# Optimization experiments

Measured on AMD Instinct MI355X. Metric: run time of the kernel, lower is better.

The kernel has to match this reference:

```python
import jax, jax.numpy as jnp
import numpy as np
import math

E = 1024      # embed_dim
H = 16        # n_heads
D = E // H    # head_dim
C = 64        # chunk_size
B = 4
N = 4096
EPS = 1e-5


def _ln(x, g, b):
    m = jnp.mean(x, axis=-1, keepdims=True)
    v = jnp.mean(jnp.square(x - m), axis=-1, keepdims=True)
    return (x - m) * jax.lax.rsqrt(v + EPS) * g + b


def _chunked_attention(q, k, v):
    # q, k, v: [B, H, N, D] -> sliding-window causal attention, window = 2*C
    b, h, n, d = q.shape
    pad = (-n) % C
    if pad:
        q = jnp.pad(q, ((0, 0), (0, 0), (0, pad), (0, 0)))
        k = jnp.pad(k, ((0, 0), (0, 0), (0, pad), (0, 0)))
        v = jnp.pad(v, ((0, 0), (0, 0), (0, pad), (0, 0)))
    np_ = n + pad
    nc = np_ // C
    qc = q.reshape(b, h, nc, C, d)
    kc = k.reshape(b, h, nc, C, d)
    vc = v.reshape(b, h, nc, C, d)
    # prepend a zero chunk, window = [prev_chunk ; current_chunk] -> [b,h,nc,2C,d]
    kp = jnp.pad(kc, ((0, 0), (0, 0), (1, 0), (0, 0), (0, 0)))
    vp = jnp.pad(vc, ((0, 0), (0, 0), (1, 0), (0, 0), (0, 0)))
    kw = jnp.concatenate([kp[:, :, :-1], kp[:, :, 1:]], axis=3)
    vw = jnp.concatenate([vp[:, :, :-1], vp[:, :, 1:]], axis=3)
    scale = 1.0 / math.sqrt(d)
    scores = jnp.einsum('bhncd,bhnwd->bhncw', qc, kw) * scale  # [b,h,nc,C,2C]
    # causal: position i in chunk may attend window slots j <= C + i
    i = jnp.arange(C)[:, None]
    j = jnp.arange(2 * C)[None, :]
    mask = j <= (C + i)
    scores = jnp.where(mask, scores, -jnp.inf)
    attn = jax.nn.softmax(scores, axis=-1)
    out = jnp.einsum('bhncw,bhnwd->bhncd', attn, vw)
    out = out.reshape(b, h, np_, d)
    return out[:, :, :n]


def setup_inputs() -> dict:
    key = jax.random.key(0)
    ks = jax.random.split(key, 20)
    s = 0.02
    inp = {
        'x': jax.random.normal(ks[0], (B, N, E), jnp.float32),
        'p_i_plus_1': jax.random.normal(ks[1], (B, N, E), jnp.float32),
        'wq': jax.random.normal(ks[2], (E, E), jnp.float32) * s,
        'bq': jnp.zeros((E,), jnp.float32),
        'wk': jax.random.normal(ks[3], (E, E), jnp.float32) * s,
        'bk': jnp.zeros((E,), jnp.float32),
        'wv': jax.random.normal(ks[4], (E, E), jnp.float32) * s,
        'bv': jnp.zeros((E,), jnp.float32),
        'wo': jax.random.normal(ks[5], (E, E), jnp.float32) * s,
        'bo': jnp.zeros((E,), jnp.float32),
        'w1': jax.random.normal(ks[6], (E, 4 * E), jnp.float32) * s,
        'b1': jnp.zeros((4 * E,), jnp.float32),
        'w2': jax.random.normal(ks[7], (4 * E, E), jnp.float32) * s,
        'b2': jnp.zeros((E,), jnp.float32),
        'g1': jnp.ones((E,), jnp.float32),
        'beta1': jnp.zeros((E,), jnp.float32),
        'g2': jnp.ones((E,), jnp.float32),
        'beta2': jnp.zeros((E,), jnp.float32),
    }
    return inp


def reference(x, p_i_plus_1, wq, bq, wk, bk, wv, bv, wo, bo,
              w1, b1, w2, b2, g1, beta1, g2, beta2):
    b, n, e = x.shape
    resid = x
    xn = _ln(x, g1, beta1)
    q = (xn @ wq + bq).reshape(b, n, H, D).transpose(0, 2, 1, 3)
    k = (xn @ wk + bk).reshape(b, n, H, D).transpose(0, 2, 1, 3)
    v = (xn @ wv + bv).reshape(b, n, H, D).transpose(0, 2, 1, 3)
    ao = _chunked_attention(q, k, v)               # [b,H,n,D]
    ao = ao.transpose(0, 2, 1, 3).reshape(b, n, e)
    x1 = resid + (ao @ wo + bo)
    h = _ln(x1, g2, beta2)
    ff = jax.nn.gelu(h @ w1 + b1, approximate=False) @ w2 + b2
    x2 = x1 + ff
    pc_loss = jnp.mean(jnp.square(x2 - p_i_plus_1))
    return (x2, x2, pc_loss)
```

## Files before the change

kernel.cpp:

```cpp
#include <hip/hip_runtime.h>
#include <hip/hip_bf16.h>

#define Ecst 1024
#define Hh 16
#define Dd 64
#define Cc_ 64
#define Bb 4
#define Nn_ 4096
#define Mrows (Bb*Nn_)
#define BNE (Bb*Nn_*Ecst)

typedef __attribute__((ext_vector_type(4))) float f32x4;
typedef __attribute__((ext_vector_type(8))) short short8;
typedef __attribute__((ext_vector_type(4))) unsigned short ushort4v;

__device__ __forceinline__ float bf2f(unsigned short u) {
    union { float f; unsigned int i; } x; x.i = ((unsigned int)u) << 16; return x.f;
}
__device__ __forceinline__ unsigned short f2bf(float f) {
    __hip_bfloat16 h = __float2bfloat16(f);
    return *reinterpret_cast<unsigned short*>(&h);
}
__device__ __forceinline__ void glds16(const unsigned short* g, unsigned short* l) {
    __builtin_amdgcn_global_load_lds(
        (const __attribute__((address_space(1))) unsigned int*)g,
        (__attribute__((address_space(3))) unsigned int*)l, 16, 0, 0);
}

__global__ __launch_bounds__(256) void transpose_cast(const float* __restrict__ in,
                                                      unsigned short* __restrict__ out,
                                                      int R, int Cc) {
    __shared__ float tile[32][33];
    int c0 = blockIdx.x * 32, r0 = blockIdx.y * 32;
    int tx = threadIdx.x, ty = threadIdx.y;
#pragma unroll
    for (int i = 0; i < 4; ++i)
        tile[ty + i*8][tx] = in[(size_t)(r0 + ty + i*8) * Cc + c0 + tx];
    __syncthreads();
#pragma unroll
    for (int i = 0; i < 4; ++i)
        out[(size_t)(c0 + ty + i*8) * R + r0 + tx] = f2bf(tile[tx][ty + i*8]);
}

__global__ __launch_bounds__(256) void ln_kernel(const float* __restrict__ x,
                                                 const float* __restrict__ g,
                                                 const float* __restrict__ be,
                                                 unsigned short* __restrict__ out) {
    int row = blockIdx.x, tid = threadIdx.x;
    const float4 xv = *(const float4*)(x + (size_t)row * Ecst + tid * 4);
    float s = xv.x + xv.y + xv.z + xv.w;
    float q = xv.x*xv.x + xv.y*xv.y + xv.z*xv.z + xv.w*xv.w;
#pragma unroll
    for (int off = 32; off; off >>= 1) { s += __shfl_xor(s, off); q += __shfl_xor(q, off); }
    __shared__ float sb[8];
    int lane = tid & 63, w = tid >> 6;
    if (lane == 0) { sb[w] = s; sb[4 + w] = q; }
    __syncthreads();
    s = sb[0] + sb[1] + sb[2] + sb[3];
    q = sb[4] + sb[5] + sb[6] + sb[7];
    float mean = s * (1.0f / Ecst);
    float var  = q * (1.0f / Ecst) - mean * mean;
    float rs = rsqrtf(var + 1e-5f);
    ushort4v o;
    const float* xp = (const float*)&xv;
#pragma unroll
    for (int u = 0; u < 4; ++u) {
        float val = (xp[u] - mean) * rs * g[tid*4+u] + be[tid*4+u];
        o[u] = f2bf(val);
    }
    *(ushort4v*)(out + (size_t)row * Ecst + tid * 4) = o;
}

template<int EPI>
__global__ __launch_bounds__(256) void gemm_bt(const unsigned short* __restrict__ A,
                                               const unsigned short* __restrict__ Bt,
                                               const float* __restrict__ bias,
                                               int M, int Nc, int K,
                                               unsigned short* __restrict__ Ob,
                                               float* __restrict__ Of,
                                               const float* __restrict__ resid,
                                               float* __restrict__ Of2) {
    __shared__ unsigned short As[128 * 32];
    __shared__ unsigned short Bs[128 * 32];
    const int tid = threadIdx.x;
    const int lane = tid & 63, wid = tid >> 6;
    const int wm = wid >> 1, wn = wid & 1;
    const int tm = blockIdx.x * 128, tn = blockIdx.y * 128;
    const int s0 = wid * 128 + lane;
    const int s1 = s0 + 64;
    const unsigned short* gA0 = A  + (size_t)(tm + (s0 >> 2)) * K + (s0 & 3) * 8;
    const unsigned short* gA1 = A  + (size_t)(tm + (s1 >> 2)) * K + (s1 & 3) * 8;
    const unsigned short* gB0 = Bt + (size_t)(tn + (s0 >> 2)) * K + (s0 & 3) * 8;
    const unsigned short* gB1 = Bt + (size_t)(tn + (s1 >> 2)) * K + (s1 & 3) * 8;
    unsigned short* lA0 = As + (size_t)wid * 1024;
    unsigned short* lA1 = As + (size_t)wid * 1024 + 512;
    unsigned short* lB0 = Bs + (size_t)wid * 1024;
    unsigned short* lB1 = Bs + (size_t)wid * 1024 + 512;
    f32x4 acc[4][4] = {};
    for (int kt = 0; kt < K; kt += 32) {
        glds16(gA0 + kt, lA0);
        glds16(gA1 + kt, lA1);
        glds16(gB0 + kt, lB0);
        glds16(gB1 + kt, lB1);
        __syncthreads();
        short8 af[4], bfr[4];
#pragma unroll
        for (int mi = 0; mi < 4; ++mi)
            af[mi] = *(const short8*)(As + (wm*64 + mi*16 + (lane & 15)) * 32 + (lane >> 4) * 8);
#pragma unroll
        for (int ni = 0; ni < 4; ++ni)
            bfr[ni] = *(const short8*)(Bs + (wn*64 + ni*16 + (lane & 15)) * 32 + (lane >> 4) * 8);
#pragma unroll
        for (int mi = 0; mi < 4; ++mi)
#pragma unroll
            for (int ni = 0; ni < 4; ++ni)
                acc[mi][ni] = __builtin_amdgcn_mfma_f32_16x16x32_bf16(af[mi], bfr[ni], acc[mi][ni], 0, 0, 0);
        __syncthreads();
    }
    const int col = lane & 15, rquad = (lane >> 4) * 4;
#pragma unroll
    for (int mi = 0; mi < 4; ++mi) {
#pragma unroll
        for (int ni = 0; ni < 4; ++ni) {
            int gcol = tn + wn*64 + ni*16 + col;
            float bia = bias[gcol];
#pragma unroll
            for (int j = 0; j < 4; ++j) {
                int grow = tm + wm*64 + mi*16 + rquad + j;
                size_t idx = (size_t)grow * Nc + gcol;
                float val = acc[mi][ni][j] + bia;
                if (EPI == 0) {
                    Ob[idx] = f2bf(val);
                } else if (EPI == 1) {
                    Of[idx] = resid[idx] + val;
                } else if (EPI == 2) {
                    Ob[idx] = f2bf(0.5f * val * (1.0f + erff(val * 0.70710678118654752f)));
                } else {
                    float v2 = resid[idx] + val;
                    Of[idx] = v2; Of2[idx] = v2;
                }
            }
        }
    }
}

#define QS_OFF(r,d0) ((r)*64  + ((((d0)>>3) ^ ((r)&7))  << 3))
#define KS_OFF(j,d0) ((j)*64  + ((((d0)>>3) ^ ((j)&7))  << 3))
#define VT_OFF(d,j0) ((d)*128 + ((((j0)>>3) ^ ((d)&15)) << 3))
#define PS_OFF(r,c0) ((r)*128 + ((((c0)>>3) ^ ((r)&15)) << 3))
__global__ __launch_bounds__(256) void attn_mfma(const unsigned short* __restrict__ q,
                                                 const unsigned short* __restrict__ k,
                                                 const unsigned short* __restrict__ v,
                                                 unsigned short* __restrict__ ao) {
    __shared__ unsigned short qs[64 * 64];
    __shared__ unsigned short ks[128 * 64];
    __shared__ unsigned short vT[64 * 128];
    __shared__ unsigned short ps[64 * 128];
    int bx = blockIdx.x;
    int c = bx & 63, h = (bx >> 6) & 15, b = bx >> 10;
    int tid = threadIdx.x, lane = tid & 63, w = tid >> 6;
    size_t base = ((size_t)b * Nn_ + c * 64) * Ecst + h * 64;
#pragma unroll
    for (int i = 0; i < 2; ++i) {
        int cc = tid + i * 256;
        int row = cc >> 3, d0 = (cc & 7) * 8;
        short8 vq = *(const short8*)(q + base + (size_t)row * Ecst + d0);
        *(short8*)(qs + QS_OFF(row, d0)) = vq;
    }
#pragma unroll
    for (int i = 0; i < 4; ++i) {
        int cc = tid + i * 256;
        int j = cc >> 3, d0 = (cc & 7) * 8;
        short8 vk = {}; short8 vv = {};
        if (c > 0 || j >= 64) {
            int srcRow = (j < 64) ? (c - 1) * 64 + j : c * 64 + (j - 64);
            size_t sb = ((size_t)b * Nn_ + srcRow) * Ecst + h * 64 + d0;
            vk = *(const short8*)(k + sb);
            vv = *(const short8*)(v + sb);
        }
        *(short8*)(ks + KS_OFF(j, d0)) = vk;
#pragma unroll
        for (int u = 0; u < 8; ++u)
            vT[VT_OFF(d0 + u, j & ~7) + (j & 7)] = ((unsigned short*)&vv)[u];
    }
    __syncthreads();
    const int rA = w * 16 + (lane & 15);
    const int ksel = (lane >> 4) * 8;
    f32x4 s[8] = {};
#pragma unroll
    for (int kk = 0; kk < 2; ++kk) {
        short8 aq = *(const short8*)(qs + QS_OFF(rA, kk * 32 + ksel));
#pragma unroll
        for (int ni = 0; ni < 8; ++ni) {
            int j = ni * 16 + (lane & 15);
            short8 bk = *(const short8*)(ks + KS_OFF(j, kk * 32 + ksel));
            s[ni] = __builtin_amdgcn_mfma_f32_16x16x32_bf16(aq, bk, s[ni], 0, 0, 0);
        }
    }
    float inv[4];
    const int rq = (lane >> 4) * 4;
#pragma unroll
    for (int jr = 0; jr < 4; ++jr) {
        int i = w * 16 + rq + jr;
        float vals[8]; float mx = -1e30f;
#pragma unroll
        for (int ni = 0; ni < 8; ++ni) {
            int colw = ni * 16 + (lane & 15);
            bool valid = (colw < 64) || (colw - 64 <= i);
            float vv = valid ? s[ni][jr] * 0.125f : -1e30f;
            vals[ni] = vv;
            mx = fmaxf(mx, vv);
        }
#pragma unroll
        for (int off = 8; off; off >>= 1) mx = fmaxf(mx, __shfl_xor(mx, off));
        float sum = 0.f;
#pragma unroll
        for (int ni = 0; ni < 8; ++ni) {
            float e = (vals[ni] > -1e29f) ? __expf(vals[ni] - mx) : 0.f;
            vals[ni] = e; sum += e;
        }
#pragma unroll
        for (int off = 8; off; off >>= 1) sum += __shfl_xor(sum, off);
        inv[jr] = 1.0f / sum;
        int r = w * 16 + rq + jr;
#pragma unroll
        for (int ni = 0; ni < 8; ++ni) {
            int colw = ni * 16 + (lane & 15);
            ps[PS_OFF(r, colw & ~7) + (colw & 7)] = f2bf(vals[ni]);
        }
    }
    __syncthreads();
    f32x4 o[4] = {};
#pragma unroll
    for (int kk = 0; kk < 4; ++kk) {
        short8 ap = *(const short8*)(ps + PS_OFF(rA, kk * 32 + ksel));
#pragma unroll
        for (int ni = 0; ni < 4; ++ni) {
            int d = ni * 16 + (lane & 15);
            short8 bv = *(const short8*)(vT + VT_OFF(d, kk * 32 + ksel));
            o[ni] = __builtin_amdgcn_mfma_f32_16x16x32_bf16(ap, bv, o[ni], 0, 0, 0);
        }
    }
#pragma unroll
    for (int ni = 0; ni < 4; ++ni) {
#pragma unroll
        for (int jr = 0; jr < 4; ++jr) {
            int row = w * 16 + rq + jr;
            int d = ni * 16 + (lane & 15);
            ao[base + (size_t)row * Ecst + d] = f2bf(o[ni][jr] * inv[jr]);
        }
    }
}

__global__ __launch_bounds__(256) void loss_partial(const float* __restrict__ x2,
                                                    const float* __restrict__ p,
                                                    float* __restrict__ partials) {
    float s = 0.f;
    for (size_t idx = (size_t)blockIdx.x * 256 + threadIdx.x; idx < BNE / 4; idx += (size_t)gridDim.x * 256) {
        float4 a = *(const float4*)(x2 + idx * 4);
        float4 b = *(const float4*)(p + idx * 4);
        float dx = a.x - b.x, dy = a.y - b.y, dz = a.z - b.z, dw = a.w - b.w;
        s += dx*dx + dy*dy + dz*dz + dw*dw;
    }
#pragma unroll
    for (int off = 32; off; off >>= 1) s += __shfl_xor(s, off);
    __shared__ float sb[4];
    int lane = threadIdx.x & 63, w = threadIdx.x >> 6;
    if (lane == 0) sb[w] = s;
    __syncthreads();
    if (threadIdx.x == 0) partials[blockIdx.x] = sb[0] + sb[1] + sb[2] + sb[3];
}

__global__ __launch_bounds__(256) void loss_final(const float* __restrict__ partials,
                                                  float* __restrict__ out) {
    float s = 0.f;
    for (int i = threadIdx.x; i < 2048; i += 256) s += partials[i];
#pragma unroll
    for (int off = 32; off; off >>= 1) s += __shfl_xor(s, off);
    __shared__ float sb[4];
    int lane = threadIdx.x & 63, w = threadIdx.x >> 6;
    if (lane == 0) sb[w] = s;
    __syncthreads();
    if (threadIdx.x == 0) out[0] = (sb[0] + sb[1] + sb[2] + sb[3]) * (1.0f / (float)BNE);
}

extern "C" void kernel_launch(void* const* d_in, const int* in_sizes, int n_in,
                              void* d_out, int out_size, void* d_ws, size_t ws_size,
                              hipStream_t stream) {
    const float* x     = (const float*)d_in[0];
    const float* p     = (const float*)d_in[1];
    const float* wq    = (const float*)d_in[2];
    const float* bq    = (const float*)d_in[3];
    const float* wk    = (const float*)d_in[4];
    const float* bk    = (const float*)d_in[5];
    const float* wv    = (const float*)d_in[6];
    const float* bv    = (const float*)d_in[7];
    const float* wo    = (const float*)d_in[8];
    const float* bo    = (const float*)d_in[9];
    const float* w1    = (const float*)d_in[10];
    const float* b1    = (const float*)d_in[11];
    const float* w2    = (const float*)d_in[12];
    const float* b2    = (const float*)d_in[13];
    const float* g1    = (const float*)d_in[14];
    const float* beta1 = (const float*)d_in[15];
    const float* g2    = (const float*)d_in[16];
    const float* beta2 = (const float*)d_in[17];

    char* ws = (char*)d_ws;
    size_t off = 0;
    auto alloc = [&](size_t bytes) { void* pp = ws + off; off += (bytes + 255) & ~(size_t)255; return pp; };
    unsigned short* wqT = (unsigned short*)alloc((size_t)Ecst * Ecst * 2);
    unsigned short* wkT = (unsigned short*)alloc((size_t)Ecst * Ecst * 2);
    unsigned short* wvT = (unsigned short*)alloc((size_t)Ecst * Ecst * 2);
    unsigned short* woT = (unsigned short*)alloc((size_t)Ecst * Ecst * 2);
    unsigned short* w1T = (unsigned short*)alloc((size_t)4 * Ecst * Ecst * 2);
    unsigned short* w2T = (unsigned short*)alloc((size_t)4 * Ecst * Ecst * 2);
    unsigned short* xn  = (unsigned short*)alloc((size_t)Mrows * Ecst * 2);
    unsigned short* qb  = (unsigned short*)alloc((size_t)Mrows * Ecst * 2);
    unsigned short* kb  = (unsigned short*)alloc((size_t)Mrows * Ecst * 2);
    unsigned short* vb  = (unsigned short*)alloc((size_t)Mrows * Ecst * 2);
    unsigned short* aob = (unsigned short*)alloc((size_t)Mrows * Ecst * 2);
    unsigned short* ff1 = (unsigned short*)alloc((size_t)Mrows * 4 * Ecst * 2);
    float* partials     = (float*)alloc(2048 * 4);

    float* x1 = (float*)d_out;
    float* out2 = (float*)d_out + BNE;
    float* lossp = (float*)d_out + 2 * (size_t)BNE;

    dim3 tb(32, 8);
    transpose_cast<<<dim3(32, 32),  tb, 0, stream>>>(wq, wqT, Ecst, Ecst);
    transpose_cast<<<dim3(32, 32),  tb, 0, stream>>>(wk, wkT, Ecst, Ecst);
    transpose_cast<<<dim3(32, 32),  tb, 0, stream>>>(wv, wvT, Ecst, Ecst);
    transpose_cast<<<dim3(32, 32),  tb, 0, stream>>>(wo, woT, Ecst, Ecst);
    transpose_cast<<<dim3(128, 32), tb, 0, stream>>>(w1, w1T, Ecst, 4 * Ecst);
    transpose_cast<<<dim3(32, 128), tb, 0, stream>>>(w2, w2T, 4 * Ecst, Ecst);

    ln_kernel<<<Mrows, 256, 0, stream>>>(x, g1, beta1, xn);

    dim3 gq(Mrows / 128, Ecst / 128);
    gemm_bt<0><<<gq, 256, 0, stream>>>(xn, wqT, bq, Mrows, Ecst, Ecst, qb, nullptr, nullptr, nullptr);
    gemm_bt<0><<<gq, 256, 0, stream>>>(xn, wkT, bk, Mrows, Ecst, Ecst, kb, nullptr, nullptr, nullptr);
    gemm_bt<0><<<gq, 256, 0, stream>>>(xn, wvT, bv, Mrows, Ecst, Ecst, vb, nullptr, nullptr, nullptr);

    attn_mfma<<<Bb * Hh * (Nn_ / Cc_), 256, 0, stream>>>(qb, kb, vb, aob);

    gemm_bt<1><<<gq, 256, 0, stream>>>(aob, woT, bo, Mrows, Ecst, Ecst, nullptr, x1, x, nullptr);

    ln_kernel<<<Mrows, 256, 0, stream>>>(x1, g2, beta2, xn);

    gemm_bt<2><<<dim3(Mrows / 128, 4 * Ecst / 128), 256, 0, stream>>>(xn, w1T, b1, Mrows, 4 * Ecst, Ecst, ff1, nullptr, nullptr, nullptr);

    gemm_bt<3><<<gq, 256, 0, stream>>>(ff1, w2T, b2, Mrows, Ecst, 4 * Ecst, nullptr, x1, x1, out2);

    loss_partial<<<2048, 256, 0, stream>>>((const float*)d_out, p, partials);
    loss_final<<<1, 256, 0, stream>>>(partials, lossp);
}
```

Measured before the change: 922.2 us.

## Replace GEMM with 256x256 triple-buffered tiles and fuse QKV projection

Replaces the 128x128 single-buffered GEMM with a 256x256-tile, 512-thread kernel. The new kernel uses three LDS stages of async global-to-LDS loads, swizzled LDS addressing, XCD-aware workgroup remapping and raised wave priority around the MFMA blocks. The Q, K and V projections are merged into one GEMM over a concatenated weight and bias, and attention reads from the interleaved QKV buffer. The aim is more data reuse per tile, latency hidden behind prefetch, and fewer launches. The cost is larger register and LDS use, plus a grid of only 256 blocks for the N=1024 GEMMs, which may underfill the device.

```diff
diff --git a/kernel.cpp b/kernel.cpp
--- a/kernel.cpp
+++ b/kernel.cpp
@@ -42,6 +42,14 @@
         out[(size_t)(c0 + ty + i*8) * R + r0 + tx] = f2bf(tile[tx][ty + i*8]);
 }
 
+__global__ __launch_bounds__(256) void concat3(const float* __restrict__ a,
+                                               const float* __restrict__ b,
+                                               const float* __restrict__ c,
+                                               float* __restrict__ o) {
+    int i = blockIdx.x * 256 + threadIdx.x;
+    if (i < 1024) { o[i] = a[i]; o[1024 + i] = b[i]; o[2048 + i] = c[i]; }
+}
+
 __global__ __launch_bounds__(256) void ln_kernel(const float* __restrict__ x,
                                                  const float* __restrict__ g,
                                                  const float* __restrict__ be,
@@ -71,62 +79,99 @@
     *(ushort4v*)(out + (size_t)row * Ecst + tid * 4) = o;
 }
 
-template<int EPI>
-__global__ __launch_bounds__(256) void gemm_bt(const unsigned short* __restrict__ A,
-                                               const unsigned short* __restrict__ Bt,
-                                               const float* __restrict__ bias,
-                                               int M, int Nc, int K,
-                                               unsigned short* __restrict__ Ob,
-                                               float* __restrict__ Of,
-                                               const float* __restrict__ resid,
-                                               float* __restrict__ Of2) {
-    __shared__ unsigned short As[128 * 32];
-    __shared__ unsigned short Bs[128 * 32];
+template<int EPI, int K>
+__global__ __launch_bounds__(512, 2) void gemm256(const unsigned short* __restrict__ A,
+                                                  const unsigned short* __restrict__ Bt,
+                                                  const float* __restrict__ bias,
+                                                  int Nc, int nbn,
+                                                  unsigned short* __restrict__ Ob,
+                                                  float* __restrict__ Of,
+                                                  const float* __restrict__ resid,
+                                                  float* __restrict__ Of2) {
+    extern __shared__ unsigned short smem[];
+    unsigned short* const As0 = smem;
+    unsigned short* const As1 = smem + 8192;
+    unsigned short* const As2 = smem + 16384;
+    unsigned short* const Bs0 = smem + 24576;
+    unsigned short* const Bs1 = smem + 32768;
+    unsigned short* const Bs2 = smem + 40960;
+    constexpr int NT = K / 32;
     const int tid = threadIdx.x;
     const int lane = tid & 63, wid = tid >> 6;
-    const int wm = wid >> 1, wn = wid & 1;
-    const int tm = blockIdx.x * 128, tn = blockIdx.y * 128;
-    const int s0 = wid * 128 + lane;
-    const int s1 = s0 + 64;
-    const unsigned short* gA0 = A  + (size_t)(tm + (s0 >> 2)) * K + (s0 & 3) * 8;
-    const unsigned short* gA1 = A  + (size_t)(tm + (s1 >> 2)) * K + (s1 & 3) * 8;
-    const unsigned short* gB0 = Bt + (size_t)(tn + (s0 >> 2)) * K + (s0 & 3) * 8;
-    const unsigned short* gB1 = Bt + (size_t)(tn + (s1 >> 2)) * K + (s1 & 3) * 8;
-    unsigned short* lA0 = As + (size_t)wid * 1024;
-    unsigned short* lA1 = As + (size_t)wid * 1024 + 512;
-    unsigned short* lB0 = Bs + (size_t)wid * 1024;
-    unsigned short* lB1 = Bs + (size_t)wid * 1024 + 512;
-    f32x4 acc[4][4] = {};
-    for (int kt = 0; kt < K; kt += 32) {
-        glds16(gA0 + kt, lA0);
-        glds16(gA1 + kt, lA1);
-        glds16(gB0 + kt, lB0);
-        glds16(gB1 + kt, lB1);
-        __syncthreads();
-        short8 af[4], bfr[4];
-#pragma unroll
-        for (int mi = 0; mi < 4; ++mi)
-            af[mi] = *(const short8*)(As + (wm*64 + mi*16 + (lane & 15)) * 32 + (lane >> 4) * 8);
-#pragma unroll
-        for (int ni = 0; ni < 4; ++ni)
-            bfr[ni] = *(const short8*)(Bs + (wn*64 + ni*16 + (lane & 15)) * 32 + (lane >> 4) * 8);
-#pragma unroll
-        for (int mi = 0; mi < 4; ++mi)
-#pragma unroll
-            for (int ni = 0; ni < 4; ++ni)
-                acc[mi][ni] = __builtin_amdgcn_mfma_f32_16x16x32_bf16(af[mi], bfr[ni], acc[mi][ni], 0, 0, 0);
-        __syncthreads();
-    }
-    const int col = lane & 15, rquad = (lane >> 4) * 4;
-#pragma unroll
-    for (int mi = 0; mi < 4; ++mi) {
+    const int wm = wid >> 2, wn = wid & 3;
+    const int l = lane & 15, g = lane >> 4;
+    const int nwg = gridDim.x, cpx = nwg >> 3;
+    const int orig = blockIdx.x;
+    const int wg = (orig & 7) * cpx + (orig >> 3);
+    const int tm = (wg / nbn) * 256, tn = (wg % nbn) * 256;
+    const int c0 = tid, c1 = 512 + tid;
+    const int r0 = c0 >> 2, r1 = c1 >> 2;
+    const int sg0 = (c0 & 3) ^ ((r0 >> 1) & 3);
+    const int sg1 = (c1 & 3) ^ ((r1 >> 1) & 3);
+    const size_t aO0 = (size_t)(tm + r0) * K + sg0 * 8;
+    const size_t aO1 = (size_t)(tm + r1) * K + sg1 * 8;
+    const size_t bO0 = (size_t)(tn + r0) * K + sg0 * 8;
+    const size_t bO1 = (size_t)(tn + r1) * K + sg1 * 8;
+    const int wls0 = wid * 512;
+    const int wls1 = 4096 + wid * 512;
+    auto stage = [&](int kt, unsigned short* SA, unsigned short* SB) {
+        const unsigned short* gA = A + (size_t)kt * 32;
+        const unsigned short* gB = Bt + (size_t)kt * 32;
+        glds16(gA + aO0, SA + wls0);
+        glds16(gB + bO0, SB + wls0);
+        glds16(gA + aO1, SA + wls1);
+        glds16(gB + bO1, SB + wls1);
+    };
+    const int seg = (g ^ ((l >> 1) & 3)) * 8;
+    int frA[8], frB[4];
+#pragma unroll
+    for (int mi = 0; mi < 8; ++mi) frA[mi] = (wm * 128 + mi * 16 + l) * 32 + seg;
+#pragma unroll
+    for (int ni = 0; ni < 4; ++ni) frB[ni] = (wn * 64 + ni * 16 + l) * 32 + seg;
+
+    f32x4 acc[8][4] = {};
+    stage(0, As0, Bs0);
+    stage(1, As1, Bs1);
+    asm volatile("s_waitcnt vmcnt(4)" ::: "memory");
+    __builtin_amdgcn_s_barrier();
+    __builtin_amdgcn_sched_barrier(0);
+
+#define TILEBODY(RA, RB, SA, SB) \
+    { \
+        if (t + 2 < NT) stage(t + 2, SA, SB); \
+        short8 af[8], bfr[4]; \
+        _Pragma("unroll") for (int mi = 0; mi < 8; ++mi) af[mi] = *(const short8*)(RA + frA[mi]); \
+        _Pragma("unroll") for (int ni = 0; ni < 4; ++ni) bfr[ni] = *(const short8*)(RB + frB[ni]); \
+        __builtin_amdgcn_s_setprio(1); \
+        _Pragma("unroll") for (int mi = 0; mi < 8; ++mi) \
+        _Pragma("unroll") for (int ni = 0; ni < 4; ++ni) \
+            acc[mi][ni] = __builtin_amdgcn_mfma_f32_16x16x32_bf16(af[mi], bfr[ni], acc[mi][ni], 0, 0, 0); \
+        __builtin_amdgcn_s_setprio(0); \
+        if (t + 2 < NT) { asm volatile("s_waitcnt vmcnt(4)" ::: "memory"); } \
+        else            { asm volatile("s_waitcnt vmcnt(0)" ::: "memory"); } \
+        __builtin_amdgcn_s_barrier(); \
+        __builtin_amdgcn_sched_barrier(0); \
+    }
+
+    int m3 = 0;
+    for (int t = 0; t < NT; ++t) {
+        if (m3 == 0)      TILEBODY(As0, Bs0, As2, Bs2)
+        else if (m3 == 1) TILEBODY(As1, Bs1, As0, Bs0)
+        else              TILEBODY(As2, Bs2, As1, Bs1)
+        if (++m3 == 3) m3 = 0;
+    }
+#undef TILEBODY
+
+    const int col = l, rquad = g * 4;
+#pragma unroll
+    for (int mi = 0; mi < 8; ++mi) {
 #pragma unroll
         for (int ni = 0; ni < 4; ++ni) {
-            int gcol = tn + wn*64 + ni*16 + col;
+            int gcol = tn + wn * 64 + ni * 16 + col;
             float bia = bias[gcol];
 #pragma unroll
             for (int j = 0; j < 4; ++j) {
-                int grow = tm + wm*64 + mi*16 + rquad + j;
+                int grow = tm + wm * 128 + mi * 16 + rquad + j;
                 size_t idx = (size_t)grow * Nc + gcol;
                 float val = acc[mi][ni][j] + bia;
                 if (EPI == 0) {
@@ -148,9 +193,7 @@
 #define KS_OFF(j,d0) ((j)*64  + ((((d0)>>3) ^ ((j)&7))  << 3))
 #define VT_OFF(d,j0) ((d)*128 + ((((j0)>>3) ^ ((d)&15)) << 3))
 #define PS_OFF(r,c0) ((r)*128 + ((((c0)>>3) ^ ((r)&15)) << 3))
-__global__ __launch_bounds__(256) void attn_mfma(const unsigned short* __restrict__ q,
-                                                 const unsigned short* __restrict__ k,
-                                                 const unsigned short* __restrict__ v,
+__global__ __launch_bounds__(256) void attn_mfma(const unsigned short* __restrict__ qkv,
                                                  unsigned short* __restrict__ ao) {
     __shared__ unsigned short qs[64 * 64];
     __shared__ unsigned short ks[128 * 64];
@@ -159,12 +202,14 @@
     int bx = blockIdx.x;
     int c = bx & 63, h = (bx >> 6) & 15, b = bx >> 10;
     int tid = threadIdx.x, lane = tid & 63, w = tid >> 6;
-    size_t base = ((size_t)b * Nn_ + c * 64) * Ecst + h * 64;
+    const int QKV = 3 * Ecst;
+    size_t baseq = ((size_t)b * Nn_ + c * 64) * QKV + h * 64;
+    size_t baseo = ((size_t)b * Nn_ + c * 64) * Ecst + h * 64;
 #pragma unroll
     for (int i = 0; i < 2; ++i) {
         int cc = tid + i * 256;
         int row = cc >> 3, d0 = (cc & 7) * 8;
-        short8 vq = *(const short8*)(q + base + (size_t)row * Ecst + d0);
+        short8 vq = *(const short8*)(qkv + baseq + (size_t)row * QKV + d0);
         *(short8*)(qs + QS_OFF(row, d0)) = vq;
     }
 #pragma unroll
@@ -174,9 +219,9 @@
         short8 vk = {}; short8 vv = {};
         if (c > 0 || j >= 64) {
             int srcRow = (j < 64) ? (c - 1) * 64 + j : c * 64 + (j - 64);
-            size_t sb = ((size_t)b * Nn_ + srcRow) * Ecst + h * 64 + d0;
-            vk = *(const short8*)(k + sb);
-            vv = *(const short8*)(v + sb);
+            size_t sb = ((size_t)b * Nn_ + srcRow) * QKV + h * 64 + d0;
+            vk = *(const short8*)(qkv + sb + 1024);
+            vv = *(const short8*)(qkv + sb + 2048);
         }
         *(short8*)(ks + KS_OFF(j, d0)) = vk;
 #pragma unroll
@@ -247,7 +292,7 @@
         for (int jr = 0; jr < 4; ++jr) {
             int row = w * 16 + rq + jr;
             int d = ni * 16 + (lane & 15);
-            ao[base + (size_t)row * Ecst + d] = f2bf(o[ni][jr] * inv[jr]);
+            ao[baseo + (size_t)row * Ecst + d] = f2bf(o[ni][jr] * inv[jr]);
         }
     }
 }
@@ -309,48 +354,49 @@
     char* ws = (char*)d_ws;
     size_t off = 0;
     auto alloc = [&](size_t bytes) { void* pp = ws + off; off += (bytes + 255) & ~(size_t)255; return pp; };
-    unsigned short* wqT = (unsigned short*)alloc((size_t)Ecst * Ecst * 2);
-    unsigned short* wkT = (unsigned short*)alloc((size_t)Ecst * Ecst * 2);
-    unsigned short* wvT = (unsigned short*)alloc((size_t)Ecst * Ecst * 2);
-    unsigned short* woT = (unsigned short*)alloc((size_t)Ecst * Ecst * 2);
-    unsigned short* w1T = (unsigned short*)alloc((size_t)4 * Ecst * Ecst * 2);
-    unsigned short* w2T = (unsigned short*)alloc((size_t)4 * Ecst * Ecst * 2);
-    unsigned short* xn  = (unsigned short*)alloc((size_t)Mrows * Ecst * 2);
-    unsigned short* qb  = (unsigned short*)alloc((size_t)Mrows * Ecst * 2);
-    unsigned short* kb  = (unsigned short*)alloc((size_t)Mrows * Ecst * 2);
-    unsigned short* vb  = (unsigned short*)alloc((size_t)Mrows * Ecst * 2);
-    unsigned short* aob = (unsigned short*)alloc((size_t)Mrows * Ecst * 2);
-    unsigned short* ff1 = (unsigned short*)alloc((size_t)Mrows * 4 * Ecst * 2);
-    float* partials     = (float*)alloc(2048 * 4);
+    unsigned short* wqkvT = (unsigned short*)alloc((size_t)3 * Ecst * Ecst * 2);
+    unsigned short* woT  = (unsigned short*)alloc((size_t)Ecst * Ecst * 2);
+    unsigned short* w1T  = (unsigned short*)alloc((size_t)4 * Ecst * Ecst * 2);
+    unsigned short* w2T  = (unsigned short*)alloc((size_t)4 * Ecst * Ecst * 2);
+    float* bqkv          = (float*)alloc(3 * Ecst * 4);
+    unsigned short* xn   = (unsigned short*)alloc((size_t)Mrows * Ecst * 2);
+    unsigned short* qkv  = (unsigned short*)alloc((size_t)Mrows * 3 * Ecst * 2);
+    unsigned short* aob  = (unsigned short*)alloc((size_t)Mrows * Ecst * 2);
+    unsigned short* ff1  = (unsigned short*)alloc((size_t)Mrows * 4 * Ecst * 2);
+    float* partials      = (float*)alloc(2048 * 4);
 
     float* x1 = (float*)d_out;
     float* out2 = (float*)d_out + BNE;
     float* lossp = (float*)d_out + 2 * (size_t)BNE;
 
+    const int SMEM = 96 * 1024;
+    hipFuncSetAttribute((const void*)gemm256<0, 1024>, hipFuncAttributeMaxDynamicSharedMemorySize, SMEM);
+    hipFuncSetAttribute((const void*)gemm256<1, 1024>, hipFuncAttributeMaxDynamicSharedMemorySize, SMEM);
+    hipFuncSetAttribute((const void*)gemm256<2, 1024>, hipFuncAttributeMaxDynamicSharedMemorySize, SMEM);
+    hipFuncSetAttribute((const void*)gemm256<3, 4096>, hipFuncAttributeMaxDynamicSharedMemorySize, SMEM);
+
     dim3 tb(32, 8);
-    transpose_cast<<<dim3(32, 32),  tb, 0, stream>>>(wq, wqT, Ecst, Ecst);
-    transpose_cast<<<dim3(32, 32),  tb, 0, stream>>>(wk, wkT, Ecst, Ecst);
-    transpose_cast<<<dim3(32, 32),  tb, 0, stream>>>(wv, wvT, Ecst, Ecst);
+    transpose_cast<<<dim3(32, 32),  tb, 0, stream>>>(wq, wqkvT, Ecst, Ecst);
+    transpose_cast<<<dim3(32, 32),  tb, 0, stream>>>(wk, wqkvT + (size_t)Ecst * Ecst, Ecst, Ecst);
+    transpose_cast<<<dim3(32, 32),  tb, 0, stream>>>(wv, wqkvT + (size_t)2 * Ecst * Ecst, Ecst, Ecst);
     transpose_cast<<<dim3(32, 32),  tb, 0, stream>>>(wo, woT, Ecst, Ecst);
     transpose_cast<<<dim3(128, 32), tb, 0, stream>>>(w1, w1T, Ecst, 4 * Ecst);
     transpose_cast<<<dim3(32, 128), tb, 0, stream>>>(w2, w2T, 4 * Ecst, Ecst);
+    concat3<<<4, 256, 0, stream>>>(bq, bk, bv, bqkv);
 
     ln_kernel<<<Mrows, 256, 0, stream>>>(x, g1, beta1, xn);
 
-    dim3 gq(Mrows / 128, Ecst / 128);
-    gemm_bt<0><<<gq, 256, 0, stream>>>(xn, wqT, bq, Mrows, Ecst, Ecst, qb, nullptr, nullptr, nullptr);
-    gemm_bt<0><<<gq, 256, 0, stream>>>(xn, wkT, bk, Mrows, Ecst, Ecst, kb, nullptr, nullptr, nullptr);
-    gemm_bt<0><<<gq, 256, 0, stream>>>(xn, wvT, bv, Mrows, Ecst, Ecst, vb, nullptr, nullptr, nullptr);
-
-    attn_mfma<<<Bb * Hh * (Nn_ / Cc_), 256, 0, stream>>>(qb, kb, vb, aob);
-
-    gemm_bt<1><<<gq, 256, 0, stream>>>(aob, woT, bo, Mrows, Ecst, Ecst, nullptr, x1, x, nullptr);
+    gemm256<0, 1024><<<64 * 12, 512, SMEM, stream>>>(xn, wqkvT, bqkv, 3 * Ecst, 12, qkv, nullptr, nullptr, nullptr);
+
+    attn_mfma<<<Bb * Hh * (Nn_ / Cc_), 256, 0, stream>>>(qkv, aob);
+
+    gemm256<1, 1024><<<64 * 4, 512, SMEM, stream>>>(aob, woT, bo, Ecst, 4, nullptr, x1, x, nullptr);
 
     ln_kernel<<<Mrows, 256, 0, stream>>>(x1, g2, beta2, xn);
 
-    gemm_bt<2><<<dim3(Mrows / 128, 4 * Ecst / 128), 256, 0, stream>>>(xn, w1T, b1, Mrows, 4 * Ecst, Ecst, ff1, nullptr, nullptr, nullptr);
-
-    gemm_bt<3><<<gq, 256, 0, stream>>>(ff1, w2T, b2, Mrows, Ecst, 4 * Ecst, nullptr, x1, x1, out2);
+    gemm256<2, 1024><<<64 * 16, 512, SMEM, stream>>>(xn, w1T, b1, 4 * Ecst, 16, ff1, nullptr, nullptr, nullptr);
+
+    gemm256<3, 4096><<<64 * 4, 512, SMEM, stream>>>(ff1, w2T, b2, Ecst, 4, nullptr, x1, x1, out2);
 
     loss_partial<<<2048, 256, 0, stream>>>((const float*)d_out, p, partials);
     loss_final<<<1, 256, 0, stream>>>(partials, lossp);
```

Result: slower. 1.695 ms (+83.8%).
